# Kernel optimization log

Measured on AMD Instinct MI355X. Metric: run time of the kernel, lower is better.

## Reference

```python
import jax, jax.numpy as jnp
import numpy as np

N = 100000
E = 800000
D = 128


def setup_inputs() -> dict:
    key = jax.random.key(0)
    k1, k2, k3, k4 = jax.random.split(key, 4)
    x = jax.random.normal(k1, (N, D), dtype=jnp.float32)
    edge_index = jax.random.randint(k2, (2, E), 0, N, dtype=jnp.int64)
    s = 1.0 / np.sqrt(D)
    W1 = jax.random.uniform(k3, (D, D), jnp.float32, -s, s)
    b1 = jnp.zeros((D,), jnp.float32)
    W2 = jax.random.uniform(k4, (D, D), jnp.float32, -s, s)
    b2 = jnp.zeros((D,), jnp.float32)
    return {"x": x, "edge_index": edge_index, "W1": W1, "b1": b1, "W2": W2, "b2": b2}


def _degree(idx, n, dtype):
    return jax.ops.segment_sum(jnp.ones(idx.shape, dtype), idx, num_segments=n)


def _graph_conv(x, row, col, W, b, residual, act):
    n = x.shape[0]
    deg_out = jnp.clip(_degree(row, n, x.dtype), 1.0)          # [N]
    x_src = x * jax.lax.rsqrt(deg_out)[:, None]                # [N, D]
    # scatter-add messages from source (row) into target (col)
    agg = jax.ops.segment_sum(x_src[row], col, num_segments=n)  # [N, D]
    out = agg @ W.T + b
    deg_in = jnp.clip(_degree(col, n, x.dtype), 1.0)
    out = out * jax.lax.rsqrt(deg_in)[:, None]
    if residual:
        out = out + x  # res_fc is Identity (in_dim == out_dim)
    if act:
        out = jax.nn.relu(out)
    return out


def reference(x, edge_index, W1, b1, W2, b2):
    row, col = edge_index[0], edge_index[1]
    # layer 1: relu + residual; layer 2 (last, encoding=False): no act, no residual
    h = _graph_conv(x, row, col, W1, b1, residual=True, act=True)
    h = _graph_conv(h, row, col, W2, b2, residual=False, act=False)
    return h
```

## Files before the change

### kernel.cpp

```cpp
#include <hip/hip_runtime.h>


#define NN 100000
#define EE 800000
#define DD 128
#define NB1 98
#define NTILE (NN / 16)

#define CC 64
#define CH (EE / CC)
#define HALF 50000
#define HWORDS 12500
#define NWORDS 25000

#define FB (EE / 256)
#define PB (NN * 32 / 256)

typedef __attribute__((ext_vector_type(8))) short short8;
typedef __attribute__((ext_vector_type(4))) float floatx4;

__device__ inline float bf2f(unsigned int u16) {
    union { unsigned int i; float f; } c;
    c.i = u16 << 16;
    return c.f;
}
__device__ inline ushort f2bf(float f) {
    union { float f; unsigned int i; } c;
    c.f = f;
    unsigned int u = c.i;
    return (ushort)((u + 0x7fffu + ((u >> 16) & 1u)) >> 16);
}

__global__ __launch_bounds__(512) void count_kernel(const int* __restrict__ row,
                                                    const int* __restrict__ col,
                                                    unsigned int* __restrict__ partial_out,
                                                    unsigned int* __restrict__ partial_in,
                                                    unsigned char* __restrict__ off_u8,
                                                    const float* __restrict__ W1,
                                                    const float* __restrict__ W2,
                                                    ushort* __restrict__ wb1,
                                                    ushort* __restrict__ wb2) {
    __shared__ unsigned int h[HWORDS];
    for (int i = threadIdx.x; i < HWORDS; i += 512) h[i] = 0;
    if (threadIdx.x < 32) {
        int i = blockIdx.x * 32 + threadIdx.x;
        const float* W = (i < 4096) ? W1 : W2;
        ushort* wb = (i < 4096) ? wb1 : wb2;
        int j = i & 4095;
        float4 v = ((const float4*)W)[j];
        ushort4 o;
        o.x = f2bf(v.x); o.y = f2bf(v.y); o.z = f2bf(v.z); o.w = f2bf(v.w);
        ((ushort4*)wb)[j] = o;
    }
    __syncthreads();

    const int kind = blockIdx.x >> 7;
    const int r = (blockIdx.x >> 6) & 1;
    const int c = blockIdx.x & 63;
    const int* __restrict__ idx = kind ? row : col;
    const int base = c * CH;
    const int lo = r * HALF;

    for (int t = threadIdx.x; t < CH; t += 512) {
        const int e = base + t;
        const unsigned int d = (unsigned int)(idx[e] - lo);
        if (d < (unsigned int)HALF) {
            const int sh = 8 * (d & 3);
            unsigned int old = atomicAdd(&h[d >> 2], 1u << sh);
            if (kind == 0) off_u8[e] = (unsigned char)((old >> sh) & 0xffu);
        }
    }
    __syncthreads();

    unsigned int* dst = (kind ? partial_out : partial_in) + c * NWORDS + r * HWORDS;
    for (int i = threadIdx.x; i < HWORDS; i += 512) dst[i] = h[i];
}

__global__ __launch_bounds__(256) void node_kernel(const unsigned int* __restrict__ partial_out,
                                                   const unsigned int* __restrict__ partial_in,
                                                   int* __restrict__ cnt_total,
                                                   unsigned int* __restrict__ xoff,
                                                   float* __restrict__ dinv_out,
                                                   float* __restrict__ dinv_in) {
    const int w = blockIdx.x * 256 + threadIdx.x;
    if (w >= NWORDS) return;
    unsigned int prefix = 0;
    unsigned int tot_out = 0;
#pragma unroll
    for (int c = 0; c < CC; ++c) {
        unsigned int v = partial_in[c * NWORDS + w];
        xoff[c * NWORDS + w] = prefix;
        prefix += v;
        tot_out += partial_out[c * NWORDS + w];
    }
    int4 ct;
    float4 fi, fo;
#pragma unroll
    for (int j = 0; j < 4; ++j) {
        int din  = (int)((prefix  >> (8 * j)) & 0xffu);
        int dout = (int)((tot_out >> (8 * j)) & 0xffu);
        ((int*)&ct)[j]   = din;
        ((float*)&fi)[j] = rsqrtf((float)max(din, 1));
        ((float*)&fo)[j] = rsqrtf((float)max(dout, 1));
    }
    ((int4*)cnt_total)[w] = ct;
    ((float4*)dinv_in)[w] = fi;
    ((float4*)dinv_out)[w] = fo;
}

__global__ __launch_bounds__(256) void scan1_kernel(const int* __restrict__ cnt,
                                                    int* __restrict__ excl,
                                                    int* __restrict__ bsums) {
    __shared__ int tmp[256];
    const int t = threadIdx.x;
    const int base = blockIdx.x * 1024 + t * 4;
    int a[4];
#pragma unroll
    for (int q = 0; q < 4; ++q) a[q] = (base + q < NN) ? cnt[base + q] : 0;
    int s = a[0] + a[1] + a[2] + a[3];
    tmp[t] = s;
    __syncthreads();
    for (int off = 1; off < 256; off <<= 1) {
        int v = 0;
        if (t >= off) v = tmp[t - off];
        __syncthreads();
        tmp[t] += v;
        __syncthreads();
    }
    int excl_s = tmp[t] - s;
    if (t == 255) bsums[blockIdx.x] = tmp[t];
    int run = excl_s;
#pragma unroll
    for (int q = 0; q < 4; ++q) {
        if (base + q < NN) excl[base + q] = run;
        run += a[q];
    }
}

__global__ __launch_bounds__(256) void scan2_kernel(int* __restrict__ bsums, int nb) {
    __shared__ int tmp[256];
    const int t = threadIdx.x;
    int s = (t < nb) ? bsums[t] : 0;
    tmp[t] = s;
    __syncthreads();
    for (int off = 1; off < 256; off <<= 1) {
        int v = 0;
        if (t >= off) v = tmp[t - off];
        __syncthreads();
        tmp[t] += v;
        __syncthreads();
    }
    if (t < nb) bsums[t] = tmp[t] - s;
}


__global__ __launch_bounds__(256) void fill_prescale_kernel(const int* __restrict__ row,
                                                            const int* __restrict__ col,
                                                            const int* __restrict__ excl,
                                                            const int* __restrict__ bsums,
                                                            const unsigned char* __restrict__ xoff_u8,
                                                            const unsigned char* __restrict__ off_u8,
                                                            int* __restrict__ srcs,
                                                            const float* __restrict__ x,
                                                            const float* __restrict__ dinv_out,
                                                            ushort* __restrict__ xb) {
    if (blockIdx.x < FB) {
        int e = blockIdx.x * 256 + threadIdx.x;
        const int cl = col[e];
        const int c = e / CH;
        const int rs = excl[cl] + bsums[cl >> 10];
        srcs[rs + (int)xoff_u8[(size_t)c * NN + cl] + (int)off_u8[e]] = row[e];
    } else {
        int idx = (blockIdx.x - FB) * 256 + threadIdx.x;
        int n = idx >> 5;
        float s = dinv_out[n];
        float4 v = ((const float4*)x)[idx];
        ushort4 o;
        o.x = f2bf(v.x * s);
        o.y = f2bf(v.y * s);
        o.z = f2bf(v.z * s);
        o.w = f2bf(v.w * s);
        ((ushort4*)xb)[idx] = o;
    }
}

__global__ __launch_bounds__(256) void gather_kernel(const ushort* __restrict__ src,
                                                     const int* __restrict__ excl,
                                                     const int* __restrict__ bsums,
                                                     const int* __restrict__ srcs,
                                                     ushort* __restrict__ agg) {
    const int node = blockIdx.x * 16 + (threadIdx.x >> 4);
    const int lane = threadIdx.x & 15;
    if (node >= NN) return;
    int p = excl[node] + bsums[node >> 10];
    const int end = (node + 1 < NN) ? excl[node + 1] + bsums[(node + 1) >> 10] : EE;
    float a0 = 0.f, a1 = 0.f, a2 = 0.f, a3 = 0.f;
    float a4 = 0.f, a5 = 0.f, a6 = 0.f, a7 = 0.f;

#define ACCUM(V)                                     \
    do {                                             \
        a0 += bf2f((V).x & 0xffffu);                 \
        a1 += bf2f((V).x >> 16);                     \
        a2 += bf2f((V).y & 0xffffu);                 \
        a3 += bf2f((V).y >> 16);                     \
        a4 += bf2f((V).z & 0xffffu);                 \
        a5 += bf2f((V).z >> 16);                     \
        a6 += bf2f((V).w & 0xffffu);                 \
        a7 += bf2f((V).w >> 16);                     \
    } while (0)

    for (; p + 3 < end; p += 4) {
        int s0 = srcs[p];
        int s1 = srcs[p + 1];
        int s2 = srcs[p + 2];
        int s3 = srcs[p + 3];
        uint4 v0 = ((const uint4*)(src + (size_t)s0 * DD))[lane];
        uint4 v1 = ((const uint4*)(src + (size_t)s1 * DD))[lane];
        uint4 v2 = ((const uint4*)(src + (size_t)s2 * DD))[lane];
        uint4 v3 = ((const uint4*)(src + (size_t)s3 * DD))[lane];
        ACCUM(v0); ACCUM(v1); ACCUM(v2); ACCUM(v3);
    }
    for (; p < end; ++p) {
        int s0 = srcs[p];
        uint4 v0 = ((const uint4*)(src + (size_t)s0 * DD))[lane];
        ACCUM(v0);
    }
#undef ACCUM

    uint4 o;
    o.x = (unsigned int)f2bf(a0) | ((unsigned int)f2bf(a1) << 16);
    o.y = (unsigned int)f2bf(a2) | ((unsigned int)f2bf(a3) << 16);
    o.z = (unsigned int)f2bf(a4) | ((unsigned int)f2bf(a5) << 16);
    o.w = (unsigned int)f2bf(a6) | ((unsigned int)f2bf(a7) << 16);
    ((uint4*)(agg + (size_t)node * DD))[lane] = o;
}

template <bool L1>
__global__ __launch_bounds__(256) void gemm_ep(const ushort* __restrict__ agg,
                                               const ushort* __restrict__ wb,
                                               const float* __restrict__ bias,
                                               const float* __restrict__ dinv_in,
                                               const float* __restrict__ dinv_out,
                                               const float* __restrict__ x,
                                               ushort* __restrict__ hs,
                                               float* __restrict__ out) {
    __shared__ ushort Ws[128 * 136];
    {
        int j = threadIdx.x >> 1;
        int k0 = (threadIdx.x & 1) * 64;
        const uint4* wp = (const uint4*)(wb + (size_t)j * DD + k0);
        uint4* dst = (uint4*)(Ws + j * 136 + k0);
#pragma unroll
        for (int q = 0; q < 8; ++q) dst[q] = wp[q];
    }
    __syncthreads();

    const int wave = threadIdx.x >> 6;
    const int lane = threadIdx.x & 63;
    const int tile = blockIdx.x * 4 + wave;
    if (tile >= NTILE) return;
    const int mi = lane & 15;
    const int quad = lane >> 4;
    const int m0 = tile * 16;

    floatx4 acc[8];
#pragma unroll
    for (int t = 0; t < 8; ++t) acc[t] = (floatx4){0.f, 0.f, 0.f, 0.f};

    const ushort* ap = agg + (size_t)(m0 + mi) * DD + quad * 8;
#pragma unroll
    for (int s = 0; s < 4; ++s) {
        short8 a = *(const short8*)(ap + s * 32);
#pragma unroll
        for (int t = 0; t < 8; ++t) {
            short8 b = *(const short8*)(Ws + (t * 16 + mi) * 136 + s * 32 + quad * 8);
            acc[t] = __builtin_amdgcn_mfma_f32_16x16x32_bf16(a, b, acc[t], 0, 0, 0);
        }
    }

    float dv[4], dov[4];
#pragma unroll
    for (int i = 0; i < 4; ++i) {
        int r = m0 + quad * 4 + i;
        dv[i] = dinv_in[r];
        if (L1) dov[i] = dinv_out[r];
    }
#pragma unroll
    for (int t = 0; t < 8; ++t) {
        int c = t * 16 + mi;
        float bv = bias[c];
#pragma unroll
        for (int i = 0; i < 4; ++i) {
            int r = m0 + quad * 4 + i;
            float o = (acc[t][i] + bv) * dv[i];
            if (L1) {
                o += x[(size_t)r * DD + c];
                o = fmaxf(o, 0.f);
                hs[(size_t)r * DD + c] = f2bf(o * dov[i]);
            } else {
                out[(size_t)r * DD + c] = o;
            }
        }
    }
}

extern "C" void kernel_launch(void* const* d_in, const int* in_sizes, int n_in,
                              void* d_out, int out_size, void* d_ws, size_t ws_size,
                              hipStream_t stream) {
    const float* x  = (const float*)d_in[0];
    const int*   ei = (const int*)d_in[1];
    const float* W1 = (const float*)d_in[2];
    const float* b1 = (const float*)d_in[3];
    const float* W2 = (const float*)d_in[4];
    const float* b2 = (const float*)d_in[5];
    float* out = (float*)d_out;

    const int* row = ei;
    const int* col = ei + EE;

    ushort* agg     = (ushort*)d_ws;
    ushort* xb      = agg + (size_t)NN * DD;
    float* dinv_out = (float*)(xb + (size_t)NN * DD);
    float* dinv_in  = dinv_out + NN;
    int*   cnt      = (int*)(dinv_in + NN);
    int*   excl     = cnt + NN;
    int*   srcs     = excl + NN;
    int*   bsums    = srcs + EE;
    ushort* wb1     = (ushort*)(bsums + 256);
    ushort* wb2     = wb1 + DD * DD;

    unsigned char* off_u8      = (unsigned char*)agg;
    unsigned int*  partial_in  = (unsigned int*)(off_u8 + EE);
    unsigned int*  partial_out = partial_in + CC * NWORDS;
    unsigned int*  xoff        = partial_out + CC * NWORDS;

    count_kernel<<<256, 512, 0, stream>>>(row, col, partial_out, partial_in, off_u8,
                                          W1, W2, wb1, wb2);
    node_kernel<<<(NWORDS + 255) / 256, 256, 0, stream>>>(partial_out, partial_in, cnt, xoff,
                                                          dinv_out, dinv_in);
    scan1_kernel<<<NB1, 256, 0, stream>>>(cnt, excl, bsums);
    scan2_kernel<<<1, 256, 0, stream>>>(bsums, NB1);

    fill_prescale_kernel<<<FB + PB, 256, 0, stream>>>(row, col, excl, bsums,
                                                      (const unsigned char*)xoff, off_u8, srcs,
                                                      x, dinv_out, xb);

    gather_kernel<<<(NN + 15) / 16, 256, 0, stream>>>(xb, excl, bsums, srcs, agg);
    gemm_ep<true><<<(NTILE + 3) / 4, 256, 0, stream>>>(agg, wb1, b1, dinv_in, dinv_out, x,
                                                       xb, nullptr);

    gather_kernel<<<(NN + 15) / 16, 256, 0, stream>>>(xb, excl, bsums, srcs, agg);
    gemm_ep<false><<<(NTILE + 3) / 4, 256, 0, stream>>>(agg, wb2, b2, dinv_in, nullptr, nullptr,
                                                        nullptr, out);
}
```

Measured before the change: 264.1 us.

## Fuse neighbor gather with MFMA GEMM epilogue through shared memory tile

Merges the gather kernel and the GEMM+epilogue kernel into one kernel per layer. Each block aggregates 16 nodes into an LDS tile, then four waves each compute two 16-column MFMA tiles, reading weights directly from global/L2 instead of staging the full weight matrix in LDS. This removes the bf16 aggregate round-trip to global memory and two launches. In exchange, each block re-reads weight fragments from cache, and the layer-1 output now goes to a separate buffer (h1) rather than overwriting xb.

Result: slower. 273.8 us (+3.7%).

```diff
diff --git a/kernel.cpp b/kernel.cpp
--- a/kernel.cpp
+++ b/kernel.cpp
@@ -184,18 +184,28 @@
     }
 }
 
-__global__ __launch_bounds__(256) void gather_kernel(const ushort* __restrict__ src,
-                                                     const int* __restrict__ excl,
-                                                     const int* __restrict__ bsums,
-                                                     const int* __restrict__ srcs,
-                                                     ushort* __restrict__ agg) {
-    const int node = blockIdx.x * 16 + (threadIdx.x >> 4);
-    const int lane = threadIdx.x & 15;
-    if (node >= NN) return;
-    int p = excl[node] + bsums[node >> 10];
-    const int end = (node + 1 < NN) ? excl[node + 1] + bsums[(node + 1) >> 10] : EE;
-    float a0 = 0.f, a1 = 0.f, a2 = 0.f, a3 = 0.f;
-    float a4 = 0.f, a5 = 0.f, a6 = 0.f, a7 = 0.f;
+template <bool L1>
+__global__ __launch_bounds__(256) void gather_gemm(const ushort* __restrict__ src,
+                                                   const int* __restrict__ excl,
+                                                   const int* __restrict__ bsums,
+                                                   const int* __restrict__ srcs,
+                                                   const ushort* __restrict__ wb,
+                                                   const float* __restrict__ bias,
+                                                   const float* __restrict__ dinv_in,
+                                                   const float* __restrict__ dinv_out,
+                                                   const float* __restrict__ x,
+                                                   ushort* __restrict__ hs,
+                                                   float* __restrict__ out) {
+    __shared__ ushort At[16 * 136];
+
+    {
+        const int nl = threadIdx.x >> 4;
+        const int lane16 = threadIdx.x & 15;
+        const int node = blockIdx.x * 16 + nl;
+        int p = excl[node] + bsums[node >> 10];
+        const int end = (node + 1 < NN) ? excl[node + 1] + bsums[(node + 1) >> 10] : EE;
+        float a0 = 0.f, a1 = 0.f, a2 = 0.f, a3 = 0.f;
+        float a4 = 0.f, a5 = 0.f, a6 = 0.f, a7 = 0.f;
 
 #define ACCUM(V)                                     \
     do {                                             \
@@ -209,73 +219,51 @@
         a7 += bf2f((V).w >> 16);                     \
     } while (0)
 
-    for (; p + 3 < end; p += 4) {
-        int s0 = srcs[p];
-        int s1 = srcs[p + 1];
-        int s2 = srcs[p + 2];
-        int s3 = srcs[p + 3];
-        uint4 v0 = ((const uint4*)(src + (size_t)s0 * DD))[lane];
-        uint4 v1 = ((const uint4*)(src + (size_t)s1 * DD))[lane];
-        uint4 v2 = ((const uint4*)(src + (size_t)s2 * DD))[lane];
-        uint4 v3 = ((const uint4*)(src + (size_t)s3 * DD))[lane];
-        ACCUM(v0); ACCUM(v1); ACCUM(v2); ACCUM(v3);
-    }
-    for (; p < end; ++p) {
-        int s0 = srcs[p];
-        uint4 v0 = ((const uint4*)(src + (size_t)s0 * DD))[lane];
-        ACCUM(v0);
-    }
+        for (; p + 3 < end; p += 4) {
+            int s0 = srcs[p];
+            int s1 = srcs[p + 1];
+            int s2 = srcs[p + 2];
+            int s3 = srcs[p + 3];
+            uint4 v0 = ((const uint4*)(src + (size_t)s0 * DD))[lane16];
+            uint4 v1 = ((const uint4*)(src + (size_t)s1 * DD))[lane16];
+            uint4 v2 = ((const uint4*)(src + (size_t)s2 * DD))[lane16];
+            uint4 v3 = ((const uint4*)(src + (size_t)s3 * DD))[lane16];
+            ACCUM(v0); ACCUM(v1); ACCUM(v2); ACCUM(v3);
+        }
+        for (; p < end; ++p) {
+            int s0 = srcs[p];
+            uint4 v0 = ((const uint4*)(src + (size_t)s0 * DD))[lane16];
+            ACCUM(v0);
+        }
 #undef ACCUM
 
-    uint4 o;
-    o.x = (unsigned int)f2bf(a0) | ((unsigned int)f2bf(a1) << 16);
-    o.y = (unsigned int)f2bf(a2) | ((unsigned int)f2bf(a3) << 16);
-    o.z = (unsigned int)f2bf(a4) | ((unsigned int)f2bf(a5) << 16);
-    o.w = (unsigned int)f2bf(a6) | ((unsigned int)f2bf(a7) << 16);
-    ((uint4*)(agg + (size_t)node * DD))[lane] = o;
-}
-
-template <bool L1>
-__global__ __launch_bounds__(256) void gemm_ep(const ushort* __restrict__ agg,
-                                               const ushort* __restrict__ wb,
-                                               const float* __restrict__ bias,
-                                               const float* __restrict__ dinv_in,
-                                               const float* __restrict__ dinv_out,
-                                               const float* __restrict__ x,
-                                               ushort* __restrict__ hs,
-                                               float* __restrict__ out) {
-    __shared__ ushort Ws[128 * 136];
-    {
-        int j = threadIdx.x >> 1;
-        int k0 = (threadIdx.x & 1) * 64;
-        const uint4* wp = (const uint4*)(wb + (size_t)j * DD + k0);
-        uint4* dst = (uint4*)(Ws + j * 136 + k0);
-#pragma unroll
-        for (int q = 0; q < 8; ++q) dst[q] = wp[q];
+        uint4 o;
+        o.x = (unsigned int)f2bf(a0) | ((unsigned int)f2bf(a1) << 16);
+        o.y = (unsigned int)f2bf(a2) | ((unsigned int)f2bf(a3) << 16);
+        o.z = (unsigned int)f2bf(a4) | ((unsigned int)f2bf(a5) << 16);
+        o.w = (unsigned int)f2bf(a6) | ((unsigned int)f2bf(a7) << 16);
+        *(uint4*)(At + nl * 136 + lane16 * 8) = o;
     }
     __syncthreads();
 
     const int wave = threadIdx.x >> 6;
     const int lane = threadIdx.x & 63;
-    const int tile = blockIdx.x * 4 + wave;
-    if (tile >= NTILE) return;
     const int mi = lane & 15;
     const int quad = lane >> 4;
-    const int m0 = tile * 16;
-
-    floatx4 acc[8];
-#pragma unroll
-    for (int t = 0; t < 8; ++t) acc[t] = (floatx4){0.f, 0.f, 0.f, 0.f};
-
-    const ushort* ap = agg + (size_t)(m0 + mi) * DD + quad * 8;
+    const int m0 = blockIdx.x * 16;
+    const int t0 = wave * 2;
+
+    floatx4 acc0 = (floatx4){0.f, 0.f, 0.f, 0.f};
+    floatx4 acc1 = (floatx4){0.f, 0.f, 0.f, 0.f};
+    const ushort* ap = At + mi * 136 + quad * 8;
+    const ushort* bp = wb + (size_t)mi * DD + quad * 8;
 #pragma unroll
     for (int s = 0; s < 4; ++s) {
-        short8 a = *(const short8*)(ap + s * 32);
-#pragma unroll
-        for (int t = 0; t < 8; ++t) {
-            short8 b = *(const short8*)(Ws + (t * 16 + mi) * 136 + s * 32 + quad * 8);
-            acc[t] = __builtin_amdgcn_mfma_f32_16x16x32_bf16(a, b, acc[t], 0, 0, 0);
-        }
+        short8 a  = *(const short8*)(ap + s * 32);
+        short8 b0 = *(const short8*)(bp + (size_t)(t0 * 16) * DD + s * 32);
+        short8 b1 = *(const short8*)(bp + (size_t)(t0 * 16 + 16) * DD + s * 32);
+        acc0 = __builtin_amdgcn_mfma_f32_16x16x32_bf16(a, b0, acc0, 0, 0, 0);
+        acc1 = __builtin_amdgcn_mfma_f32_16x16x32_bf16(a, b1, acc1, 0, 0, 0);
     }
 
     float dv[4], dov[4];
@@ -286,13 +274,14 @@
         if (L1) dov[i] = dinv_out[r];
     }
 #pragma unroll
-    for (int t = 0; t < 8; ++t) {
-        int c = t * 16 + mi;
-        float bv = bias[c];
+    for (int u = 0; u < 2; ++u) {
+        const int c = (t0 + u) * 16 + mi;
+        const float bv = bias[c];
+        const floatx4 av = u ? acc1 : acc0;
 #pragma unroll
         for (int i = 0; i < 4; ++i) {
             int r = m0 + quad * 4 + i;
-            float o = (acc[t][i] + bv) * dv[i];
+            float o = (av[i] + bv) * dv[i];
             if (L1) {
                 o += x[(size_t)r * DD + c];
                 o = fmaxf(o, 0.f);
@@ -318,8 +307,8 @@
     const int* row = ei;
     const int* col = ei + EE;
 
-    ushort* agg     = (ushort*)d_ws;
-    ushort* xb      = agg + (size_t)NN * DD;
+    ushort* h1      = (ushort*)d_ws;
+    ushort* xb      = h1 + (size_t)NN * DD;
     float* dinv_out = (float*)(xb + (size_t)NN * DD);
     float* dinv_in  = dinv_out + NN;
     int*   cnt      = (int*)(dinv_in + NN);
@@ -329,7 +318,7 @@
     ushort* wb1     = (ushort*)(bsums + 256);
     ushort* wb2     = wb1 + DD * DD;
 
-    unsigned char* off_u8      = (unsigned char*)agg;
+    unsigned char* off_u8      = (unsigned char*)h1;
     unsigned int*  partial_in  = (unsigned int*)(off_u8 + EE);
     unsigned int*  partial_out = partial_in + CC * NWORDS;
     unsigned int*  xoff        = partial_out + CC * NWORDS;
@@ -345,11 +334,9 @@
                                                       (const unsigned char*)xoff, off_u8, srcs,
                                                       x, dinv_out, xb);
 
-    gather_kernel<<<(NN + 15) / 16, 256, 0, stream>>>(xb, excl, bsums, srcs, agg);
-    gemm_ep<true><<<(NTILE + 3) / 4, 256, 0, stream>>>(agg, wb1, b1, dinv_in, dinv_out, x,
-                                                       xb, nullptr);
-
-    gather_kernel<<<(NN + 15) / 16, 256, 0, stream>>>(xb, excl, bsums, srcs, agg);
-    gemm_ep<false><<<(NTILE + 3) / 4, 256, 0, stream>>>(agg, wb2, b2, dinv_in, nullptr, nullptr,
-                                                        nullptr, out);
-}
+    gather_gemm<true><<<NTILE, 256, 0, stream>>>(xb, excl, bsums, srcs, wb1, b1,
+                                                 dinv_in, dinv_out, x, h1, nullptr);
+
+    gather_gemm<false><<<NTILE, 256, 0, stream>>>(h1, excl, bsums, srcs, wb2, b2,
+                                                  dinv_in, nullptr, nullptr, nullptr, out);
+}
```
